# Kernel optimization log

Measured on AMD Instinct MI355X. Metric: run time of the kernel, lower is better.

Reference implementation:

```python
import jax, jax.numpy as jnp
import numpy as np

N = 8192
D = 2048      # input_dim
DH = 1024     # input_dim // r
DO = 1024     # output_dim

def setup_inputs() -> dict:
    key = jax.random.key(0)
    ks = jax.random.split(key, 11)
    s_in = 1.0 / np.sqrt(D)
    s_h = 1.0 / np.sqrt(DH)
    return {
        "O0": jax.random.normal(ks[0], (N, D), dtype=jnp.float32),
        "Ww": jax.random.uniform(ks[1], (DH, D), jnp.float32, -s_in, s_in),
        "Wb": jax.random.uniform(ks[2], (DH,), jnp.float32, -s_in, s_in),
        "Uw": jax.random.uniform(ks[3], (DH, D), jnp.float32, -s_in, s_in),
        "Ub": jax.random.uniform(ks[4], (DH,), jnp.float32, -s_in, s_in),
        "Hw": jax.random.uniform(ks[5], (DH, D), jnp.float32, -s_in, s_in),
        "Hb": jax.random.uniform(ks[6], (DH,), jnp.float32, -s_in, s_in),
        "fc0w": jax.random.uniform(ks[7], (D, DH), jnp.float32, -s_h, s_h),
        "fc0b": jax.random.uniform(ks[8], (D,), jnp.float32, -s_h, s_h),
        "fc1w": jax.random.uniform(ks[9], (DO, D), jnp.float32, -s_in, s_in),
        "fc1b": jax.random.uniform(ks[10], (DO,), jnp.float32, -s_in, s_in),
    }

def reference(O0, Ww, Wb, Uw, Ub, Hw, Hb, fc0w, fc0b, fc1w, fc1b):
    q = O0 @ Ww.T + Wb              # [N, DH]
    k = O0 @ Uw.T + Ub              # [N, DH]
    v = O0 @ Hw.T + Hb              # [N, DH]
    scores = q @ k.T                # [N, N], unscaled as in the original
    R1 = jax.nn.softmax(scores, axis=1)
    ctx = R1 @ v                    # [N, DH]
    O1 = O0 + (ctx @ fc0w.T + fc0b) # residual, [N, D]
    O2 = O1 @ fc1w.T + fc1b         # [N, DO]
    return (O1, O2)
```

## Files before the change

### kernel.cpp

```cpp
#include <hip/hip_runtime.h>
#include <cstdint>
#include <cstddef>

typedef _Float16 f16;
typedef _Float16 f16x8 __attribute__((ext_vector_type(8)));
typedef _Float16 f16x4 __attribute__((ext_vector_type(4)));
typedef float    f32x4 __attribute__((ext_vector_type(4)));

template <int V> struct IC { static constexpr int v = V; };

template <int CTRL>
__device__ __forceinline__ float dppf(float x) {
  union { float f; int i; } u, r;
  u.f = x;
  r.i = __builtin_amdgcn_update_dpp(0, u.i, CTRL, 0xF, 0xF, true);
  return r.f;
}

__global__ __launch_bounds__(256) void cvt_f32_f16(const float* __restrict__ in,
                                                   f16* __restrict__ out, int n) {
  int i = (blockIdx.x * 256 + threadIdx.x) * 4;
  if (i < n) {
    float4 v = *(const float4*)(in + i);
    f16x4 h; h[0] = (f16)v.x; h[1] = (f16)v.y; h[2] = (f16)v.z; h[3] = (f16)v.w;
    *(f16x4*)(out + i) = h;
  }
}

__global__ __launch_bounds__(256) void cvt5_f32_f16(
    const float* __restrict__ i0, const float* __restrict__ i1,
    const float* __restrict__ i2, const float* __restrict__ i3,
    const float* __restrict__ i4, f16* __restrict__ out, int nper) {
  const int bpr = nper >> 10;
  const int r = blockIdx.x / bpr;
  const int b = blockIdx.x - r * bpr;
  const float* in = r == 0 ? i0 : r == 1 ? i1 : r == 2 ? i2 : r == 3 ? i3 : i4;
  int i = (b * 256 + threadIdx.x) * 4;
  float4 v = *(const float4*)(in + i);
  f16x4 h; h[0] = (f16)v.x; h[1] = (f16)v.y; h[2] = (f16)v.z; h[3] = (f16)v.w;
  *(f16x4*)(out + (size_t)r * nper + i) = h;
}

__global__ __launch_bounds__(256) void transpose_f16(const f16* __restrict__ in,
                                                     int ldi,
                                                     f16* __restrict__ out,
                                                     int R, int C) {
  __shared__ f16 tile[64][65];
  const int r0 = blockIdx.y * 64, c0 = blockIdx.x * 64;
  const int t = threadIdx.x;
#pragma unroll
  for (int p = 0; p < 2; p++) {
    int s = t + p * 256;
    int r = s >> 3, q = s & 7;
    const int kl = ((r & 3) << 4) + (r >> 2);
    f16x8 v = *(const f16x8*)(in + (size_t)(r0 + kl) * ldi + c0 + q * 8);
#pragma unroll
    for (int e = 0; e < 8; e++) tile[r][q * 8 + e] = v[e];
  }
  __syncthreads();
#pragma unroll
  for (int p = 0; p < 2; p++) {
    int s = t + p * 256;
    int r = s >> 3, q = s & 7;
    f16x8 v;
#pragma unroll
    for (int e = 0; e < 8; e++) v[e] = tile[q * 8 + e][r];
    *(f16x8*)(out + (size_t)(c0 + r) * R + r0 + q * 8) = v;
  }
}

template <int MODE>
__global__ __launch_bounds__(512, 2) void gemm256(
    const f16* __restrict__ A, const f16* __restrict__ B,
    int M, int N, int K, int lda, int ldb,
    const float* __restrict__ bias,
    f16* __restrict__ outH, int ldo,
    float* __restrict__ statsM, float* __restrict__ statsS, int sld,
    const float* __restrict__ alphaT,
    const float* __restrict__ resid, int ldr,
    float* __restrict__ outF, int ldof) {
  __shared__ f16 lA[2][2][128 * 64];
  __shared__ f16 lB[2][2][128 * 64];
  __shared__ float lAl[2][256];

  const int t = threadIdx.x;
  const int wave = t >> 6, lane = t & 63;
  const int wr = wave >> 2, wc = wave & 3;
  const int quad = lane >> 4, l16 = lane & 15;
  const int rc = lane >> 3;
  const int kcs = (lane & 7) ^ rc;

  const int nwg = gridDim.x * gridDim.y;
  const int bid = blockIdx.y * gridDim.x + blockIdx.x;
  const int sb = (bid & 7) * (nwg >> 3) + (bid >> 3);
  const int bx = sb % gridDim.x, by = sb / gridDim.x;
  const int m0 = by * 256, n0 = bx * 256;
  const int nk = K >> 6;

  const f16* Abase = A + (size_t)m0 * lda;
  const f16* Bbase = B + (size_t)n0 * ldb;

  auto stageA = [&](int tau, int h) {
    if (tau >= nk) return;
    const f16* src = Abase + (size_t)(h * 128 + rc) * lda + tau * 64 + kcs * 8;
    f16* dstu = &lA[tau & 1][h][0];
#pragma unroll
    for (int j = 0; j < 2; j++) {
      const int sl = j * 8 + wave;
      __builtin_amdgcn_global_load_lds(
          (const __attribute__((address_space(1))) void*)(src + (size_t)sl * 8 * lda),
          (__attribute__((address_space(3))) void*)(dstu + sl * 512), 16, 0, 0);
    }
  };
  auto stageB = [&](int tau, int h) {
    if (tau >= nk) return;
    const f16* src = Bbase + (size_t)(h * 128 + rc) * ldb + tau * 64 + kcs * 8;
    f16* dstu = &lB[tau & 1][h][0];
#pragma unroll
    for (int j = 0; j < 2; j++) {
      const int sl = j * 8 + wave;
      __builtin_amdgcn_global_load_lds(
          (const __attribute__((address_space(1))) void*)(src + (size_t)sl * 8 * ldb),
          (__attribute__((address_space(3))) void*)(dstu + sl * 512), 16, 0, 0);
    }
  };
  auto stageAl = [&](int tau) {
    if constexpr (MODE == 2) {
      if (tau >= nk) return;
      __builtin_amdgcn_global_load_lds(
          (const __attribute__((address_space(1))) void*)(alphaT + (size_t)tau * M + m0 + lane * 4),
          (__attribute__((address_space(3))) void*)(&lAl[tau & 1][0]), 16, 0, 0);
    }
  };

  f32x4 acc[2][4][2][2];
#pragma unroll
  for (int mh = 0; mh < 2; mh++)
#pragma unroll
    for (int i = 0; i < 4; i++)
#pragma unroll
      for (int nh = 0; nh < 2; nh++)
#pragma unroll
        for (int j = 0; j < 2; j++)
#pragma unroll
          for (int e = 0; e < 4; e++) acc[mh][i][nh][j][e] = 0.0f;

  f16x8 af[4][2];
  f16x8 bf[2][2][2];

  auto readA = [&](auto BUFC, auto MHC) {
    constexpr int buf = decltype(BUFC)::v;
    constexpr int mh = decltype(MHC)::v;
#pragma unroll
    for (int i = 0; i < 4; i++) {
      const int r = i * 32 + wr * 16 + l16;
#pragma unroll
      for (int s = 0; s < 2; s++) {
        const int p = ((s * 4 + quad) ^ (l16 & 7)) * 8;
        af[i][s] = *(const f16x8*)(&lA[buf][mh][r * 64 + p]);
      }
      if constexpr (MODE == 2) {
        const f16 ah = (f16)lAl[buf][mh * 128 + r];
        af[i][0] = af[i][0] * ah;
        af[i][1] = af[i][1] * ah;
      }
    }
  };
  auto readB = [&](auto BUFC, auto NHC) {
    constexpr int buf = decltype(BUFC)::v;
    constexpr int nh = decltype(NHC)::v;
    const int hb = wc >> 1;
#pragma unroll
    for (int j = 0; j < 2; j++) {
      const int r = (wc & 1) * 64 + nh * 32 + j * 16 + l16;
#pragma unroll
      for (int s = 0; s < 2; s++) {
        const int p = ((s * 4 + quad) ^ (l16 & 7)) * 8;
        bf[nh][j][s] = *(const f16x8*)(&lB[buf][hb][r * 64 + p]);
      }
    }
  };
  auto mfmaQ = [&](auto MHC, auto NHC) {
    constexpr int mh = decltype(MHC)::v;
    constexpr int nh = decltype(NHC)::v;
    __builtin_amdgcn_s_setprio(1);
#pragma unroll
    for (int i = 0; i < 4; i++)
#pragma unroll
      for (int j = 0; j < 2; j++)
#pragma unroll
        for (int s = 0; s < 2; s++)
          acc[mh][i][nh][j] = __builtin_amdgcn_mfma_f32_16x16x32_f16(
              af[i][s], bf[nh][j][s], acc[mh][i][nh][j], 0, 0, 0);
    __builtin_amdgcn_s_setprio(0);
  };

  auto tile4 = [&](auto BUFC, int tt, bool dr) {
    readA(BUFC, IC<0>{});
    readB(BUFC, IC<0>{});
    stageA(tt + 1, 1);
    stageAl(tt + 1);
    __builtin_amdgcn_s_barrier();
    asm volatile("s_waitcnt lgkmcnt(0)" ::: "memory");
    mfmaQ(IC<0>{}, IC<0>{});
    __builtin_amdgcn_s_barrier();
    readB(BUFC, IC<1>{});
    stageA(tt + 2, 0);
    __builtin_amdgcn_s_barrier();
    asm volatile("s_waitcnt lgkmcnt(0)" ::: "memory");
    mfmaQ(IC<0>{}, IC<1>{});
    __builtin_amdgcn_s_barrier();
    readA(BUFC, IC<1>{});
    stageB(tt + 2, 0);
    __builtin_amdgcn_s_barrier();
    asm volatile("s_waitcnt lgkmcnt(0)" ::: "memory");
    mfmaQ(IC<1>{}, IC<1>{});
    __builtin_amdgcn_s_barrier();
    stageB(tt + 2, 1);
    __builtin_amdgcn_s_barrier();
    mfmaQ(IC<1>{}, IC<0>{});
    if (dr) { asm volatile("s_waitcnt vmcnt(0)" ::: "memory"); }
    else    { asm volatile("s_waitcnt vmcnt(6)" ::: "memory"); }
    __builtin_amdgcn_s_barrier();
  };

  stageA(0, 0); stageB(0, 0); stageB(0, 1); stageA(0, 1);
  stageAl(0);
  stageA(1, 0); stageB(1, 0); stageB(1, 1);
  asm volatile("s_waitcnt vmcnt(6)" ::: "memory");
  __builtin_amdgcn_s_barrier();

  for (int tt = 0; tt < nk; tt += 2) {
    const bool dr = (tt + 2 >= nk);
    tile4(IC<0>{}, tt, dr);
    tile4(IC<1>{}, tt + 1, dr);
  }

  const int colb = n0 + wc * 64 + l16;
  float bv[4];
  if constexpr (MODE == 0 || MODE == 3 || MODE == 4) {
#pragma unroll
    for (int c = 0; c < 4; c++) bv[c] = bias[colb + c * 16];
  }
#pragma unroll
  for (int mh = 0; mh < 2; mh++) {
#pragma unroll
    for (int i = 0; i < 4; i++) {
#pragma unroll
      for (int e = 0; e < 4; e++) {
        const int gr = m0 + mh * 128 + i * 32 + wr * 16 + quad * 4 + e;
        const float v0 = acc[mh][i][0][0][e];
        const float v1 = acc[mh][i][0][1][e];
        const float v2 = acc[mh][i][1][0][e];
        const float v3 = acc[mh][i][1][1][e];
        if constexpr (MODE == 1) {
          float mx = fmaxf(fmaxf(v0, v1), fmaxf(v2, v3));
          mx = fmaxf(mx, dppf<0xB1>(mx));
          mx = fmaxf(mx, dppf<0x4E>(mx));
          mx = fmaxf(mx, __shfl_xor(mx, 4));
          mx = fmaxf(mx, __shfl_xor(mx, 8));
          float e0 = __expf(v0 - mx);
          float e1 = __expf(v1 - mx);
          float e2 = __expf(v2 - mx);
          float e3 = __expf(v3 - mx);
          float sm = (e0 + e1) + (e2 + e3);
          sm += dppf<0xB1>(sm);
          sm += dppf<0x4E>(sm);
          sm += __shfl_xor(sm, 4);
          sm += __shfl_xor(sm, 8);
          if (l16 == 0) {
            statsM[(size_t)gr * sld + (bx * 4 + wc)] = mx;
            statsS[(size_t)gr * sld + (bx * 4 + wc)] = sm;
          }
          f16x4 pk;
          pk[0] = (f16)e0; pk[1] = (f16)e1; pk[2] = (f16)e2; pk[3] = (f16)e3;
          *(f16x4*)(outH + (size_t)gr * ldo + n0 + wc * 64 + l16 * 4) = pk;
        } else if constexpr (MODE == 0) {
          f16* rp = outH + (size_t)gr * ldo + colb;
          rp[0]  = (f16)(v0 + bv[0]);
          rp[16] = (f16)(v1 + bv[1]);
          rp[32] = (f16)(v2 + bv[2]);
          rp[48] = (f16)(v3 + bv[3]);
        } else if constexpr (MODE == 2) {
          f16* rp = outH + (size_t)gr * ldo + colb;
          rp[0]  = (f16)v0;
          rp[16] = (f16)v1;
          rp[32] = (f16)v2;
          rp[48] = (f16)v3;
        } else if constexpr (MODE == 3) {
          float* rf = outF + (size_t)gr * ldof + colb;
          const float* rr = resid + (size_t)gr * ldr + colb;
          f16* rh = outH + (size_t)gr * ldo + colb;
          float o0 = v0 + bv[0] + rr[0];
          float o1 = v1 + bv[1] + rr[16];
          float o2 = v2 + bv[2] + rr[32];
          float o3 = v3 + bv[3] + rr[48];
          rf[0] = o0; rf[16] = o1; rf[32] = o2; rf[48] = o3;
          rh[0] = (f16)o0; rh[16] = (f16)o1; rh[32] = (f16)o2; rh[48] = (f16)o3;
        } else {
          float* rf = outF + (size_t)gr * ldof + colb;
          rf[0]  = v0 + bv[0];
          rf[16] = v1 + bv[1];
          rf[32] = v2 + bv[2];
          rf[48] = v3 + bv[3];
        }
      }
    }
  }
}

template <int MODE>
__global__ __launch_bounds__(512, 2) void gemmN128(
    const f16* __restrict__ A, const f16* __restrict__ B,
    int M, int N, int K, int lda, int ldb,
    const float* __restrict__ bias,
    f16* __restrict__ outH, int ldo,
    const float* __restrict__ alphaT,
    float* __restrict__ outF, int ldof) {
  __shared__ f16 lA[2][2][128 * 64];
  __shared__ f16 lB[2][128 * 64];
  __shared__ float lAl[2][256];

  const int t = threadIdx.x;
  const int wave = t >> 6, lane = t & 63;
  const int wr = wave >> 1, wc = wave & 1;
  const int quad = lane >> 4, l16 = lane & 15;
  const int rc = lane >> 3;
  const int kcs = (lane & 7) ^ rc;

  const int nwg = gridDim.x * gridDim.y;
  const int bid = blockIdx.y * gridDim.x + blockIdx.x;
  const int sb = (bid & 7) * (nwg >> 3) + (bid >> 3);
  const int bx = sb % gridDim.x, by = sb / gridDim.x;
  const int m0 = by * 256, n0 = bx * 128;
  const int nk = K >> 6;

  const f16* Abase = A + (size_t)m0 * lda;
  const f16* Bbase = B + (size_t)n0 * ldb;

  auto stageA = [&](int tau, int h) {
    if (tau >= nk) return;
    const f16* src = Abase + (size_t)(h * 128 + rc) * lda + tau * 64 + kcs * 8;
    f16* dstu = &lA[tau & 1][h][0];
#pragma unroll
    for (int j = 0; j < 2; j++) {
      const int sl = j * 8 + wave;
      __builtin_amdgcn_global_load_lds(
          (const __attribute__((address_space(1))) void*)(src + (size_t)sl * 8 * lda),
          (__attribute__((address_space(3))) void*)(dstu + sl * 512), 16, 0, 0);
    }
  };
  auto stageB = [&](int tau) {
    if (tau >= nk) return;
    const f16* src = Bbase + (size_t)rc * ldb + tau * 64 + kcs * 8;
    f16* dstu = &lB[tau & 1][0];
#pragma unroll
    for (int j = 0; j < 2; j++) {
      const int sl = j * 8 + wave;
      __builtin_amdgcn_global_load_lds(
          (const __attribute__((address_space(1))) void*)(src + (size_t)sl * 8 * ldb),
          (__attribute__((address_space(3))) void*)(dstu + sl * 512), 16, 0, 0);
    }
  };
  auto stageAl = [&](int tau) {
    if constexpr (MODE == 2) {
      if (tau >= nk) return;
      __builtin_amdgcn_global_load_lds(
          (const __attribute__((address_space(1))) void*)(alphaT + (size_t)tau * M + m0 + lane * 4),
          (__attribute__((address_space(3))) void*)(&lAl[tau & 1][0]), 16, 0, 0);
    }
  };

  f32x4 acc[4][2][2];
#pragma unroll
  for (int i = 0; i < 4; i++)
#pragma unroll
    for (int nh = 0; nh < 2; nh++)
#pragma unroll
      for (int j = 0; j < 2; j++)
#pragma unroll
        for (int e = 0; e < 4; e++) acc[i][nh][j][e] = 0.0f;

  f16x8 af[4][2];
  f16x8 bf[2][2][2];
  const int ha = wr >> 1;

  auto readA = [&](auto BUFC) {
    constexpr int buf = decltype(BUFC)::v;
#pragma unroll
    for (int i = 0; i < 4; i++) {
      const int r = (wr & 1) * 64 + i * 16 + l16;
#pragma unroll
      for (int s = 0; s < 2; s++) {
        const int p = ((s * 4 + quad) ^ (l16 & 7)) * 8;
        af[i][s] = *(const f16x8*)(&lA[buf][ha][r * 64 + p]);
      }
      if constexpr (MODE == 2) {
        const f16 ah = (f16)lAl[buf][wr * 64 + i * 16 + l16];
        af[i][0] = af[i][0] * ah;
        af[i][1] = af[i][1] * ah;
      }
    }
  };
  auto readB = [&](auto BUFC, auto NHC) {
    constexpr int buf = decltype(BUFC)::v;
    constexpr int nh = decltype(NHC)::v;
#pragma unroll
    for (int j = 0; j < 2; j++) {
      const int r = wc * 64 + nh * 32 + j * 16 + l16;
#pragma unroll
      for (int s = 0; s < 2; s++) {
        const int p = ((s * 4 + quad) ^ (l16 & 7)) * 8;
        bf[nh][j][s] = *(const f16x8*)(&lB[buf][r * 64 + p]);
      }
    }
  };
  auto mfmaQ = [&](auto NHC) {
    constexpr int nh = decltype(NHC)::v;
    __builtin_amdgcn_s_setprio(1);
#pragma unroll
    for (int i = 0; i < 4; i++)
#pragma unroll
      for (int j = 0; j < 2; j++)
#pragma unroll
        for (int s = 0; s < 2; s++)
          acc[i][nh][j] = __builtin_amdgcn_mfma_f32_16x16x32_f16(
              af[i][s], bf[nh][j][s], acc[i][nh][j], 0, 0, 0);
    __builtin_amdgcn_s_setprio(0);
  };

  auto tile2 = [&](auto BUFC, int tt, bool dr) {
    readA(BUFC);
    readB(BUFC, IC<0>{});
    readB(BUFC, IC<1>{});
    stageA(tt + 1, 1);
    stageAl(tt + 1);
    __builtin_amdgcn_s_barrier();
    asm volatile("s_waitcnt lgkmcnt(0)" ::: "memory");
    mfmaQ(IC<0>{});
    __builtin_amdgcn_s_barrier();
    stageA(tt + 2, 0);
    stageB(tt + 2);
    __builtin_amdgcn_s_barrier();
    mfmaQ(IC<1>{});
    if (dr) { asm volatile("s_waitcnt vmcnt(0)" ::: "memory"); }
    else    { asm volatile("s_waitcnt vmcnt(4)" ::: "memory"); }
    __builtin_amdgcn_s_barrier();
  };

  stageA(0, 0); stageB(0); stageA(0, 1); stageAl(0);
  stageA(1, 0); stageB(1);
  asm volatile("s_waitcnt vmcnt(4)" ::: "memory");
  __builtin_amdgcn_s_barrier();

  for (int tt = 0; tt < nk; tt += 2) {
    const bool dr = (tt + 2 >= nk);
    tile2(IC<0>{}, tt, dr);
    tile2(IC<1>{}, tt + 1, dr);
  }

  float bv[2][2];
  if constexpr (MODE == 0 || MODE == 4) {
#pragma unroll
    for (int nh = 0; nh < 2; nh++)
#pragma unroll
      for (int j = 0; j < 2; j++)
        bv[nh][j] = bias[n0 + wc * 64 + nh * 32 + j * 16 + l16];
  }
#pragma unroll
  for (int i = 0; i < 4; i++) {
#pragma unroll
    for (int e = 0; e < 4; e++) {
      const int gr = m0 + wr * 64 + i * 16 + quad * 4 + e;
#pragma unroll
      for (int nh = 0; nh < 2; nh++) {
#pragma unroll
        for (int j = 0; j < 2; j++) {
          const int col = n0 + wc * 64 + nh * 32 + j * 16 + l16;
          const float v = acc[i][nh][j][e];
          if constexpr (MODE == 2) {
            outH[(size_t)gr * ldo + col] = (f16)v;
          } else if constexpr (MODE == 0) {
            outH[(size_t)gr * ldo + col] = (f16)(v + bv[nh][j]);
          } else {
            outF[(size_t)gr * ldof + col] = v + bv[nh][j];
          }
        }
      }
    }
  }
}

__global__ __launch_bounds__(256) void alpha_from_stats(
    const float* __restrict__ sM, const float* __restrict__ sS,
    float* __restrict__ aT, int rows) {
  __shared__ float alph[128][65];
  const int t = threadIdx.x;
  const int r = t >> 2, j = t & 3;
  const int row = blockIdx.x * 64 + r;
  const float* pm = sM + (size_t)row * 128 + j * 32;
  const float* ps = sS + (size_t)row * 128 + j * 32;
  float mv[32];
  float mx = -1e30f;
#pragma unroll
  for (int c = 0; c < 32; c++) { mv[c] = pm[c]; mx = fmaxf(mx, mv[c]); }
  mx = fmaxf(mx, __shfl_xor(mx, 1));
  mx = fmaxf(mx, __shfl_xor(mx, 2));
  float ev[32];
  float sum = 0.0f;
#pragma unroll
  for (int c = 0; c < 32; c++) {
    ev[c] = __expf(mv[c] - mx);
    sum += ev[c] * ps[c];
  }
  sum += __shfl_xor(sum, 1);
  sum += __shfl_xor(sum, 2);
  const float rl = 1.0f / sum;
#pragma unroll
  for (int c = 0; c < 32; c++) alph[j * 32 + c][r] = ev[c] * rl;
  __syncthreads();
  const int wid = t >> 6, rr = t & 63;
#pragma unroll
  for (int c = 0; c < 32; c++) {
    const int tg = c * 4 + wid;
    aT[(size_t)tg * rows + blockIdx.x * 64 + rr] = alph[tg][rr];
  }
}

extern "C" void kernel_launch(void* const* d_in, const int* in_sizes, int n_in,
                              void* d_out, int out_size, void* d_ws, size_t ws_size,
                              hipStream_t stream) {
  const float* O0   = (const float*)d_in[0];
  const float* Ww   = (const float*)d_in[1];
  const float* Wb   = (const float*)d_in[2];
  const float* Uw   = (const float*)d_in[3];
  const float* Ub   = (const float*)d_in[4];
  const float* Hw   = (const float*)d_in[5];
  const float* Hb   = (const float*)d_in[6];
  const float* fc0w = (const float*)d_in[7];
  const float* fc0b = (const float*)d_in[8];
  const float* fc1w = (const float*)d_in[9];
  const float* fc1b = (const float*)d_in[10];

  const int N = 8192, D = 2048, DH = 1024, DO = 1024;
  const int NQKV = 3 * DH;

  char* w = (char*)d_ws;
  f16* Wwh   = (f16*)w; w += (size_t)DH * D * 2;
  f16* Uwh   = (f16*)w; w += (size_t)DH * D * 2;
  f16* Hwh   = (f16*)w; w += (size_t)DH * D * 2;
  f16* fc0wh = (f16*)w; w += (size_t)D * DH * 2;
  f16* fc1wh = (f16*)w; w += (size_t)DO * D * 2;
  float* aT  = (float*)w; w += (size_t)128 * N * 4;
  char* un = w; w += (size_t)N * DH * 2;
  float* statsM = (float*)un;
  float* statsS = statsM + (size_t)N * 128;
  f16* ctxh = (f16*)un;
  float* biasC = (float*)w; w += (size_t)NQKV * 4;
  w = (char*)(((uintptr_t)w + 255) & ~(uintptr_t)255);
  f16* Sb = (f16*)w;

  f16* oh   = (f16*)d_out;
  f16* qkv  = oh;
  f16* qh   = qkv;
  f16* kh   = qkv + DH;
  f16* vh   = qkv + 2 * DH;
  f16* O0h  = oh + (size_t)N * NQKV;
  f16* vT   = O0h + (size_t)N * D;
  f16* O1h  = Sb;

  {
    int nper = DH * D;
    cvt5_f32_f16<<<5 * (nper / 1024), 256, 0, stream>>>(
        Ww, Uw, Hw, fc0w, fc1w, Wwh, nper);
    cvt_f32_f16<<<(N * D) / 1024, 256, 0, stream>>>(O0, O0h, N * D);
    hipMemcpyAsync(biasC,          Wb, DH * 4, hipMemcpyDeviceToDevice, stream);
    hipMemcpyAsync(biasC + DH,     Ub, DH * 4, hipMemcpyDeviceToDevice, stream);
    hipMemcpyAsync(biasC + 2 * DH, Hb, DH * 4, hipMemcpyDeviceToDevice, stream);
  }

  gemmN128<0><<<dim3(NQKV / 128, N / 256), 512, 0, stream>>>(
      O0h, Wwh, N, NQKV, D, D, D, biasC, qkv, NQKV, nullptr, nullptr, 0);

  transpose_f16<<<dim3(DH / 64, N / 64), 256, 0, stream>>>(vh, NQKV, vT, N, DH);

  gemm256<1><<<dim3(N / 256, N / 256), 512, 0, stream>>>(
      qh, kh, N, N, DH, NQKV, NQKV, nullptr, Sb, N,
      statsM, statsS, 128, nullptr, nullptr, 0, nullptr, 0);

  alpha_from_stats<<<N / 64, 256, 0, stream>>>(statsM, statsS, aT, N);

  gemmN128<2><<<dim3(DH / 128, N / 256), 512, 0, stream>>>(
      Sb, vT, N, DH, N, N, N, nullptr, ctxh, DH, aT, nullptr, 0);

  gemm256<3><<<dim3(D / 256, N / 256), 512, 0, stream>>>(
      ctxh, fc0wh, N, D, DH, DH, DH, fc0b, O1h, D,
      nullptr, nullptr, 0, nullptr, O0, D, (float*)d_out, D);

  gemmN128<4><<<dim3(DO / 128, N / 256), 512, 0, stream>>>(
      O1h, fc1wh, N, DO, D, D, D, fc1b, nullptr, 0, nullptr,
      (float*)d_out + (size_t)N * D, DO);
}
```

Baseline: 763.3 us.

## Simplify GEMM main loops to single-barrier one-tile-lookahead prefetch schedule

```diff
diff --git a/kernel.cpp b/kernel.cpp
--- a/kernel.cpp
+++ b/kernel.cpp
@@ -195,45 +195,31 @@
     __builtin_amdgcn_s_setprio(0);
   };
 
-  auto tile4 = [&](auto BUFC, int tt, bool dr) {
+  auto tileGo = [&](auto BUFC, int tt) {
+    stageA(tt + 1, 0);
+    stageB(tt + 1, 0);
+    stageA(tt + 1, 1);
+    stageB(tt + 1, 1);
+    stageAl(tt + 1);
     readA(BUFC, IC<0>{});
     readB(BUFC, IC<0>{});
-    stageA(tt + 1, 1);
-    stageAl(tt + 1);
+    mfmaQ(IC<0>{}, IC<0>{});
+    readB(BUFC, IC<1>{});
+    mfmaQ(IC<0>{}, IC<1>{});
+    readA(BUFC, IC<1>{});
+    mfmaQ(IC<1>{}, IC<1>{});
+    mfmaQ(IC<1>{}, IC<0>{});
+    asm volatile("s_waitcnt vmcnt(0)" ::: "memory");
     __builtin_amdgcn_s_barrier();
-    asm volatile("s_waitcnt lgkmcnt(0)" ::: "memory");
-    mfmaQ(IC<0>{}, IC<0>{});
-    __builtin_amdgcn_s_barrier();
-    readB(BUFC, IC<1>{});
-    stageA(tt + 2, 0);
-    __builtin_amdgcn_s_barrier();
-    asm volatile("s_waitcnt lgkmcnt(0)" ::: "memory");
-    mfmaQ(IC<0>{}, IC<1>{});
-    __builtin_amdgcn_s_barrier();
-    readA(BUFC, IC<1>{});
-    stageB(tt + 2, 0);
-    __builtin_amdgcn_s_barrier();
-    asm volatile("s_waitcnt lgkmcnt(0)" ::: "memory");
-    mfmaQ(IC<1>{}, IC<1>{});
-    __builtin_amdgcn_s_barrier();
-    stageB(tt + 2, 1);
-    __builtin_amdgcn_s_barrier();
-    mfmaQ(IC<1>{}, IC<0>{});
-    if (dr) { asm volatile("s_waitcnt vmcnt(0)" ::: "memory"); }
-    else    { asm volatile("s_waitcnt vmcnt(6)" ::: "memory"); }
-    __builtin_amdgcn_s_barrier();
-  };
-
-  stageA(0, 0); stageB(0, 0); stageB(0, 1); stageA(0, 1);
-  stageAl(0);
-  stageA(1, 0); stageB(1, 0); stageB(1, 1);
-  asm volatile("s_waitcnt vmcnt(6)" ::: "memory");
+  };
+
+  stageA(0, 0); stageB(0, 0); stageA(0, 1); stageB(0, 1); stageAl(0);
+  asm volatile("s_waitcnt vmcnt(0)" ::: "memory");
   __builtin_amdgcn_s_barrier();
 
   for (int tt = 0; tt < nk; tt += 2) {
-    const bool dr = (tt + 2 >= nk);
-    tile4(IC<0>{}, tt, dr);
-    tile4(IC<1>{}, tt + 1, dr);
+    tileGo(IC<0>{}, tt);
+    tileGo(IC<1>{}, tt + 1);
   }
 
   const int colb = n0 + wc * 64 + l16;
@@ -429,34 +415,27 @@
     __builtin_amdgcn_s_setprio(0);
   };
 
-  auto tile2 = [&](auto BUFC, int tt, bool dr) {
+  auto tileGo = [&](auto BUFC, int tt) {
+    stageA(tt + 1, 0);
+    stageA(tt + 1, 1);
+    stageB(tt + 1);
+    stageAl(tt + 1);
     readA(BUFC);
     readB(BUFC, IC<0>{});
+    mfmaQ(IC<0>{});
     readB(BUFC, IC<1>{});
-    stageA(tt + 1, 1);
-    stageAl(tt + 1);
+    mfmaQ(IC<1>{});
+    asm volatile("s_waitcnt vmcnt(0)" ::: "memory");
     __builtin_amdgcn_s_barrier();
-    asm volatile("s_waitcnt lgkmcnt(0)" ::: "memory");
-    mfmaQ(IC<0>{});
-    __builtin_amdgcn_s_barrier();
-    stageA(tt + 2, 0);
-    stageB(tt + 2);
-    __builtin_amdgcn_s_barrier();
-    mfmaQ(IC<1>{});
-    if (dr) { asm volatile("s_waitcnt vmcnt(0)" ::: "memory"); }
-    else    { asm volatile("s_waitcnt vmcnt(4)" ::: "memory"); }
-    __builtin_amdgcn_s_barrier();
-  };
-
-  stageA(0, 0); stageB(0); stageA(0, 1); stageAl(0);
-  stageA(1, 0); stageB(1);
-  asm volatile("s_waitcnt vmcnt(4)" ::: "memory");
+  };
+
+  stageA(0, 0); stageA(0, 1); stageB(0); stageAl(0);
+  asm volatile("s_waitcnt vmcnt(0)" ::: "memory");
   __builtin_amdgcn_s_barrier();
 
   for (int tt = 0; tt < nk; tt += 2) {
-    const bool dr = (tt + 2 >= nk);
-    tile2(IC<0>{}, tt, dr);
-    tile2(IC<1>{}, tt + 1, dr);
+    tileGo(IC<0>{}, tt);
+    tileGo(IC<1>{}, tt + 1);
   }
 
   float bv[2][2];
```

Measured after the change: 772.0 us. Within noise of the previous version (+1.1%).
